# Performance work log

Measured on AMD Instinct MI355X. Metric: run time of the kernel, lower is better.

Reference implementation:

```python
import jax, jax.numpy as jnp
import numpy as np

B, N, C, H, D, K = 4, 8192, 384, 12, 2, 32
M = N // K            # 256 members per cluster
CH = C // H // 2      # 16 = q/k head dim (v gets 2*head_dim per the 6-way split)


def setup_inputs() -> dict:
    key = jax.random.key(0)
    ks = jax.random.split(key, 8)
    pos = jax.random.uniform(ks[0], (B, N, D), jnp.float32)
    feat = jax.random.normal(ks[1], (B, N, C), jnp.float32)
    # per-(b*h) row permutation of 0..N-1 -> clusters partition all tokens (cluster_mask=None path)
    perm_keys = jax.random.split(ks[2], B * H)
    member_idx = jax.vmap(lambda kk: jax.random.permutation(kk, N))(perm_keys).reshape(B * H, K, M)
    w_qkv = jax.random.normal(ks[3], (3 * C, C), jnp.float32) * (C ** -0.5)
    b_qkv = jnp.zeros((3 * C,), jnp.float32)
    w_pos = jax.random.normal(ks[4], (H, D), jnp.float32) * 0.1   # Conv1d(h*d->h, ksize 1, groups=h) weight squeezed
    b_pos = jnp.zeros((H,), jnp.float32)
    w_proj = jax.random.normal(ks[5], (C, 2 * C), jnp.float32) * ((2 * C) ** -0.5)
    b_proj = jnp.zeros((C,), jnp.float32)
    return {"pos": pos, "feat": feat, "member_idx": member_idx,
            "w_qkv": w_qkv, "b_qkv": b_qkv, "w_pos": w_pos, "b_pos": b_pos,
            "w_proj": w_proj, "b_proj": b_proj}


def reference(pos, feat, member_idx, w_qkv, b_qkv, w_pos, b_pos, w_proj, b_proj):
    b, n, c = feat.shape
    d = pos.shape[2]
    bh, k, m = member_idx.shape
    h = bh // b
    ch = c // h // 2
    scale = (c // h) ** -0.5

    # qkv projection -> (b*h, n, 6, ch)
    qkv = feat @ w_qkv.T + b_qkv                      # b n 3c
    qkv = qkv.reshape(b, n, h, 6, ch).transpose(0, 2, 1, 3, 4).reshape(bh, n, 6, ch)

    # gather cluster members -> (b*k, h, m, 6, ch)
    row = jnp.arange(bh)[:, None, None]
    g = qkv[row, member_idx]                          # bh k m 6 ch
    g = g.reshape(b, h, k, m, 6, ch).transpose(0, 2, 1, 3, 4, 5).reshape(b * k, h, m, 6, ch)
    q = g[:, :, :, 0] * scale                         # bk h m ch
    kk = g[:, :, :, 1]                                # bk h m ch
    v = g[:, :, :, 2:].reshape(b * k, h, m, 4 * ch)   # bk h m 2c_

    attn = jnp.einsum('khic,khjc->khij', q, kk)       # bk h m m (k axis = b*k)

    # positional bias: kernel-1 grouped conv is linear -> bias[i,j] = s_j - s_i + b_pos
    pos_n = pos / pos.reshape(-1, d).max(0)           # b n d
    pos_bh = jnp.repeat(pos_n, h, axis=0)             # bh n d
    pos_g = pos_bh[row, member_idx]                   # bh k m d
    pos_g = pos_g.reshape(b, h, k, m, d).transpose(0, 2, 1, 3, 4).reshape(b * k, h, m, d)
    s = jnp.einsum('khmd,hd->khm', pos_g, w_pos)      # bk h m
    pos_bias = s[:, :, None, :] - s[:, :, :, None] + b_pos[None, :, None, None]

    attn = jax.nn.softmax(attn + pos_bias, axis=-1)
    out = jnp.einsum('khij,khjc->khic', attn, v)      # bk h m 2c_

    # scatter back to original token order (member_idx is a permutation per row)
    out = out.reshape(b, k, h, m, 4 * ch).transpose(0, 2, 1, 3, 4).reshape(bh, k * m, 4 * ch)
    new_feat = jnp.zeros((bh, n, 4 * ch), out.dtype)
    new_feat = new_feat.at[jnp.arange(bh)[:, None], member_idx.reshape(bh, k * m)].set(out)
    feat2 = new_feat.reshape(b, h, n, 4 * ch).transpose(0, 2, 1, 3).reshape(b, n, 2 * c)

    return feat2 @ w_proj.T + b_proj                  # b n c
```

## Files before the change

### kernel.cpp

```cpp
#include <hip/hip_runtime.h>
#include <hip/hip_bf16.h>

#define B_  4
#define N_  8192
#define C_  384
#define H_  12
#define K_  32
#define M_  256
#define BN_ (B_*N_)
#define QKVD 1152
#define VSTR 260
#define LOG2E 1.4426950408889634f


typedef __attribute__((ext_vector_type(8)))  short  bf16x8;
typedef __attribute__((ext_vector_type(4)))  float  f32x4;
typedef __attribute__((ext_vector_type(16))) float  f32x16;
typedef __attribute__((ext_vector_type(4)))  ushort ushort4v;
typedef __attribute__((ext_vector_type(8)))  ushort ushort8v;

#define GLOBAL_AS __attribute__((address_space(1)))
#define LDS_AS    __attribute__((address_space(3)))

__device__ __forceinline__ void load_lds_16B(const ushort* g, ushort* l) {
    __builtin_amdgcn_global_load_lds((const GLOBAL_AS unsigned int*)g,
                                     (LDS_AS unsigned int*)l, 16, 0, 0);
}
__device__ __forceinline__ unsigned cvtpk_bf16(float lo, float hi) {
    unsigned r;
    asm("v_cvt_pk_bf16_f32 %0, %1, %2" : "=v"(r) : "v"(lo), "v"(hi));
    return r;
}
__device__ __forceinline__ float exp2_fast(float x) {
    float r;
    asm("v_exp_f32 %0, %1" : "=v"(r) : "v"(x));
    return r;
}
__device__ __forceinline__ float rcp_fast(float x) {
    float r;
    asm("v_rcp_f32 %0, %1" : "=v"(r) : "v"(x));
    return r;
}

#define CF_BLK 12288
#define CW_BLK 720
#define WQN 110592
#define WPN 73728
__global__ __launch_bounds__(256) void prologue_kernel(const float* __restrict__ pos,
                                                       const float* __restrict__ feat,
                                                       const float* __restrict__ wq,
                                                       const float* __restrict__ wp,
                                                       unsigned* __restrict__ pmax,
                                                       ushort* __restrict__ featb,
                                                       ushort* __restrict__ wqb,
                                                       ushort* __restrict__ wpb) {
    const int bid = blockIdx.x;
    if (bid < CF_BLK) {
        int i = bid * 256 + threadIdx.x;
        float4 a = reinterpret_cast<const float4*>(feat)[i];
        unsigned u01 = cvtpk_bf16(a.x, a.y), u23 = cvtpk_bf16(a.z, a.w);
        ushort4 o = { (ushort)(u01 & 0xffff), (ushort)(u01 >> 16),
                      (ushort)(u23 & 0xffff), (ushort)(u23 >> 16) };
        reinterpret_cast<ushort4*>(featb)[i] = o;
        return;
    }
    if (bid < CF_BLK + CW_BLK) {
        int i = (bid - CF_BLK) * 256 + threadIdx.x;
        if (i >= WQN + WPN) return;
        const float* src; ushort* dst; int j;
        if (i < WQN) { src = wq; dst = wqb; j = i; }
        else         { src = wp; dst = wpb; j = i - WQN; }
        float4 a = reinterpret_cast<const float4*>(src)[j];
        unsigned u01 = cvtpk_bf16(a.x, a.y), u23 = cvtpk_bf16(a.z, a.w);
        ushort4 o = { (ushort)(u01 & 0xffff), (ushort)(u01 >> 16),
                      (ushort)(u23 & 0xffff), (ushort)(u23 >> 16) };
        reinterpret_cast<ushort4*>(dst)[j] = o;
        return;
    }
    {
        int vb = bid - CF_BLK - CW_BLK;
        int tid = vb * 256 + threadIdx.x;
        float m0 = 0.f, m1 = 0.f;
        for (int i = tid; i < BN_; i += 8 * 256) {
            m0 = fmaxf(m0, pos[(size_t)i * 2 + 0]);
            m1 = fmaxf(m1, pos[(size_t)i * 2 + 1]);
        }
        #pragma unroll
        for (int off = 32; off; off >>= 1) {
            m0 = fmaxf(m0, __shfl_down(m0, off));
            m1 = fmaxf(m1, __shfl_down(m1, off));
        }
        __shared__ float s0[4], s1[4];
        int w = threadIdx.x >> 6;
        if ((threadIdx.x & 63) == 0) { s0[w] = m0; s1[w] = m1; }
        __syncthreads();
        if (threadIdx.x == 0) {
            for (int i = 1; i < 4; i++) { m0 = fmaxf(m0, s0[i]); m1 = fmaxf(m1, s1[i]); }
            pmax[2 * vb + 0] = __float_as_uint(m0);
            pmax[2 * vb + 1] = __float_as_uint(m1);
        }
    }
}

__global__ __launch_bounds__(512) void gemm_qkv_s(const ushort* __restrict__ A,
                                                  const ushort* __restrict__ Bw,
                                                  const float* __restrict__ bias,
                                                  ushort* __restrict__ qkv) {
    constexpr int NB = QKVD / 128;
    __shared__ ushort As[256 * 64];
    __shared__ ushort Bs[128 * 64];
    const int wgid = blockIdx.x;
    const int xcd  = wgid & 7;
    const int loc  = wgid >> 3;
    const int bm = (xcd * 16 + loc / NB) * 256;
    const int bn = (loc % NB) * 128;
    const int t = threadIdx.x;
    const int l = t & 63;
    const int wid = t >> 6;
    const int wr = wid >> 1, wc = wid & 1;
    const int fr = l & 15, fq = l >> 4;

    f32x4 zero = {0.f, 0.f, 0.f, 0.f};
    f32x4 acc[4][4];
    #pragma unroll
    for (int m = 0; m < 4; m++)
        #pragma unroll
        for (int n = 0; n < 4; n++) acc[m][n] = zero;

    for (int k0 = 0; k0 < 384; k0 += 64) {
        #pragma unroll
        for (int i = 0; i < 4; i++) {
            int elem = (i * 512 + t) * 8;
            int row = elem >> 6, kk = elem & 63;
            int kks = kk ^ ((row & 7) << 3);
            load_lds_16B(A + (size_t)(bm + row) * 384 + k0 + kks, &As[elem]);
        }
        #pragma unroll
        for (int i = 0; i < 2; i++) {
            int elem = (i * 512 + t) * 8;
            int row = elem >> 6, kk = elem & 63;
            int kks = kk ^ ((row & 7) << 3);
            load_lds_16B(Bw + (size_t)(bn + row) * 384 + k0 + kks, &Bs[elem]);
        }
        __syncthreads();
        #pragma unroll
        for (int kk = 0; kk < 64; kk += 32) {
            bf16x8 af[4], bfr[4];
            #pragma unroll
            for (int m = 0; m < 4; m++) {
                int row = wr * 64 + m * 16 + fr;
                af[m] = *reinterpret_cast<const bf16x8*>(&As[row * 64 + ((kk + fq * 8) ^ ((row & 7) << 3))]);
            }
            #pragma unroll
            for (int n = 0; n < 4; n++) {
                int row = wc * 64 + n * 16 + fr;
                bfr[n] = *reinterpret_cast<const bf16x8*>(&Bs[row * 64 + ((kk + fq * 8) ^ ((row & 7) << 3))]);
            }
            #pragma unroll
            for (int m = 0; m < 4; m++)
                #pragma unroll
                for (int n = 0; n < 4; n++)
                    acc[m][n] = __builtin_amdgcn_mfma_f32_16x16x32_bf16(af[m], bfr[n], acc[m][n], 0, 0, 0);
        }
        __syncthreads();
    }
    const int bq = bm >> 13;
    const int nbase = bm & (N_ - 1);
    #pragma unroll
    for (int n = 0; n < 4; n++) {
        int col = bn + wc * 64 + n * 16 + fr;
        int hc = col / 96, cn = col % 96;
        float bc = bias[col];
        ushort* base = qkv + ((size_t)(bq * H_ + hc) * N_ + nbase) * 96 + cn;
        #pragma unroll
        for (int m = 0; m < 4; m++) {
            #pragma unroll
            for (int r = 0; r < 4; r++) {
                int rowoff = wr * 64 + m * 16 + fq * 4 + r;
                unsigned up = cvtpk_bf16(acc[m][n][r] + bc, 0.f);
                base[(size_t)rowoff * 96] = (ushort)(up & 0xffff);
            }
        }
    }
}

__global__ __launch_bounds__(256, 2) void attn_kernel(const ushort* __restrict__ qkv,
                                                      const int* __restrict__ member_idx,
                                                      const float* __restrict__ pos,
                                                      const float* __restrict__ w_pos,
                                                      const unsigned* __restrict__ pmax_u,
                                                      ushort* __restrict__ feat2) {
    const int id = blockIdx.x;
    const int bh = (id >> 8) * 8 + (id & 7);
    const int kc = (id >> 3) & 31;
    const int b = bh / H_, h = bh % H_;
    __shared__ ushort Ks[M_ * 16];
    __shared__ ushort Vt[64 * VSTR];
    __shared__ float  SpA[M_];
    __shared__ int    Idx[M_];
    __shared__ float  dinvS[M_];

    const int t  = threadIdx.x;
    const int w  = t >> 6, l = t & 63;
    const int hi = l >> 5, ln = l & 31;
    const int* mi = member_idx + (((size_t)b * H_ + h) * K_ + kc) * M_;
    const ushort* slab = qkv + (size_t)bh * N_ * 96;
    const size_t rowbase = (size_t)b * N_;
    const float scale2 = 0.17677669529663687f * LOG2E;

    const int nq0 = mi[w * 64 + ln];
    const int nq1 = mi[w * 64 + 32 + ln];
    bf16x8 qf0 = *(const bf16x8*)(slab + (size_t)nq0 * 96 + hi * 8);
    bf16x8 qf1 = *(const bf16x8*)(slab + (size_t)nq1 * 96 + hi * 8);
    #pragma unroll
    for (int it = 0; it < 2; it++) {
        int idx = it * 256 + t;
        int row = idx >> 1, half = idx & 1;
        int n = mi[row];
        load_lds_16B(slab + (size_t)n * 96 + 16 + half * 8, &Ks[idx * 8]);
    }
    {
        int u = t >> 1, cqh = t & 1;
        int n0 = mi[2 * u], n1 = mi[2 * u + 1];
        #pragma unroll
        for (int qq = 0; qq < 2; qq++) {
            int cq = 2 * cqh + qq;
            const ushort* s0 = slab + (size_t)n0 * 96 + 32 + cq * 16;
            const ushort* s1 = slab + (size_t)n1 * 96 + 32 + cq * 16;
            union { ushort8v v; unsigned u4[4]; } v0a, v0b, v1a, v1b;
            v0a.v = *(const ushort8v*)s0;
            v0b.v = *(const ushort8v*)(s0 + 8);
            v1a.v = *(const ushort8v*)s1;
            v1b.v = *(const ushort8v*)(s1 + 8);
            #pragma unroll
            for (int iw = 0; iw < 4; iw++) {
                unsigned ea = __builtin_amdgcn_perm(v1a.u4[iw], v0a.u4[iw], 0x05040100u);
                unsigned oa = __builtin_amdgcn_perm(v1a.u4[iw], v0a.u4[iw], 0x07060302u);
                *(unsigned*)&Vt[(cq * 16 + 2 * iw)     * VSTR + 2 * u] = ea;
                *(unsigned*)&Vt[(cq * 16 + 2 * iw + 1) * VSTR + 2 * u] = oa;
                unsigned eb = __builtin_amdgcn_perm(v1b.u4[iw], v0b.u4[iw], 0x05040100u);
                unsigned ob = __builtin_amdgcn_perm(v1b.u4[iw], v0b.u4[iw], 0x07060302u);
                *(unsigned*)&Vt[(cq * 16 + 8 + 2 * iw)     * VSTR + 2 * u] = eb;
                *(unsigned*)&Vt[(cq * 16 + 8 + 2 * iw + 1) * VSTR + 2 * u] = ob;
            }
        }
    }
    {
        int n = mi[t];
        Idx[t] = n;
        float f0 = __uint_as_float(pmax_u[0]), f1 = __uint_as_float(pmax_u[1]);
        #pragma unroll
        for (int k = 1; k < 8; k++) {
            f0 = fmaxf(f0, __uint_as_float(pmax_u[2 * k + 0]));
            f1 = fmaxf(f1, __uint_as_float(pmax_u[2 * k + 1]));
        }
        float inv0 = rcp_fast(f0);
        float inv1 = rcp_fast(f1);
        float sp = pos[(rowbase + n) * 2 + 0] * inv0 * w_pos[h * 2 + 0]
                 + pos[(rowbase + n) * 2 + 1] * inv1 * w_pos[h * 2 + 1];
        int jj = t & 31, jt = t >> 5;
        int r  = (jj & 3) | ((jj >> 3) << 2);
        int hb = (jj >> 2) & 1;
        SpA[jt * 32 + hb * 16 + r] = sp * LOG2E;
    }
    __syncthreads();

    f32x16 zero16;
    #pragma unroll
    for (int i = 0; i < 16; i++) zero16[i] = 0.f;
    ushort* f2slab = feat2 + (size_t)bh * N_ * 64;

    #pragma unroll
    for (int p = 0; p < 2; p++) {
        const int qb = w * 64 + p * 32;
        const bf16x8 qf = p ? qf1 : qf0;

        f32x16 sac[8];
        __builtin_amdgcn_s_setprio(1);
        #pragma unroll
        for (int jt = 0; jt < 8; jt++) {
            bf16x8 kf = *(const bf16x8*)&Ks[(32 * jt + ln) * 16 + hi * 8];
            sac[jt] = __builtin_amdgcn_mfma_f32_32x32x16_bf16(kf, qf, zero16, 0, 0, 0);
        }
        __builtin_amdgcn_s_setprio(0);

        float mx = -3.0e38f;
        #pragma unroll
        for (int jt = 0; jt < 8; jt++) {
            f32x4 bia[4];
            #pragma unroll
            for (int q4 = 0; q4 < 4; q4++)
                bia[q4] = *(const f32x4*)&SpA[jt * 32 + hi * 16 + q4 * 4];
            #pragma unroll
            for (int r = 0; r < 16; r++)
                sac[jt][r] = fmaf(sac[jt][r], scale2, bia[r >> 2][r & 3]);
            #pragma unroll
            for (int r = 0; r < 16; r += 2)
                mx = fmaxf(mx, fmaxf(sac[jt][r], sac[jt][r + 1]));
        }
        mx = fmaxf(mx, __shfl_xor(mx, 32));
        float sum = 0.f;
        #pragma unroll
        for (int jt = 0; jt < 8; jt++)
            #pragma unroll
            for (int r = 0; r < 16; r++) {
                float pv = exp2_fast(sac[jt][r] - mx);
                sac[jt][r] = pv;
                sum += pv;
            }
        sum += __shfl_xor(sum, 32);
        float inv = rcp_fast(sum);
        if (hi == 0) dinvS[qb + ln] = inv;

        f32x16 oa0 = zero16, oa1 = zero16;
        __builtin_amdgcn_s_setprio(1);
        #pragma unroll
        for (int g = 0; g < 16; g++) {
            const int jt = g >> 1, hf = (g & 1) * 8;
            unsigned a0 = cvtpk_bf16(sac[jt][hf + 0], sac[jt][hf + 1]);
            unsigned a1 = cvtpk_bf16(sac[jt][hf + 2], sac[jt][hf + 3]);
            unsigned b0 = cvtpk_bf16(sac[jt][hf + 4], sac[jt][hf + 5]);
            unsigned b1 = cvtpk_bf16(sac[jt][hf + 6], sac[jt][hf + 7]);
            asm("v_permlane32_swap_b32 %0, %1" : "+v"(a0), "+v"(b0));
            asm("v_permlane32_swap_b32 %0, %1" : "+v"(a1), "+v"(b1));
            union { unsigned uu[4]; bf16x8 v; } pa;
            pa.uu[0] = a0; pa.uu[1] = a1; pa.uu[2] = b0; pa.uu[3] = b1;
            union { ushort4v hv[2]; bf16x8 v; } vf0, vf1;
            vf0.hv[0] = *(const ushort4v*)&Vt[ln * VSTR + g * 16 + hi * 8];
            vf0.hv[1] = *(const ushort4v*)&Vt[ln * VSTR + g * 16 + hi * 8 + 4];
            vf1.hv[0] = *(const ushort4v*)&Vt[(ln + 32) * VSTR + g * 16 + hi * 8];
            vf1.hv[1] = *(const ushort4v*)&Vt[(ln + 32) * VSTR + g * 16 + hi * 8 + 4];
            oa0 = __builtin_amdgcn_mfma_f32_32x32x16_bf16(pa.v, vf0.v, oa0, 0, 0, 0);
            oa1 = __builtin_amdgcn_mfma_f32_32x32x16_bf16(pa.v, vf1.v, oa1, 0, 0, 0);
        }
        __builtin_amdgcn_s_setprio(0);

        #pragma unroll
        for (int r = 0; r < 16; r++) {
            int crow = (r & 3) + 8 * (r >> 2) + 4 * hi;
            float dv = dinvS[qb + crow];
            int ni = Idx[qb + crow];
            unsigned up = cvtpk_bf16(oa0[r] * dv, oa1[r] * dv);
            ushort* dst = f2slab + (size_t)ni * 64 + ln;
            dst[0]  = (ushort)(up & 0xffff);
            dst[32] = (ushort)(up >> 16);
        }
    }
}

__global__ __launch_bounds__(512) void gemm_proj_s(const ushort* __restrict__ A,
                                                   const ushort* __restrict__ Bw,
                                                   const float* __restrict__ bias,
                                                   float* __restrict__ Cout) {
    constexpr int NB = C_ / 128;
    __shared__ ushort As[256 * 64];
    __shared__ ushort Bs[128 * 64];
    const int wgid = blockIdx.x;
    const int xcd  = wgid & 7;
    const int loc  = wgid >> 3;
    const int bm = (xcd * 16 + loc / NB) * 256;
    const int bn = (loc % NB) * 128;
    const int t = threadIdx.x;
    const int l = t & 63;
    const int wid = t >> 6;
    const int wr = wid >> 1, wc = wid & 1;
    const int fr = l & 15, fq = l >> 4;
    const int bq = bm >> 13;
    const int nbase = bm & (N_ - 1);

    f32x4 zero = {0.f, 0.f, 0.f, 0.f};
    f32x4 acc[4][4];
    #pragma unroll
    for (int m = 0; m < 4; m++)
        #pragma unroll
        for (int n = 0; n < 4; n++) acc[m][n] = zero;

    for (int k0 = 0; k0 < 768; k0 += 64) {
        const ushort* Aslab = A + ((size_t)(bq * H_ + (k0 >> 6)) * N_ + nbase) * 64;
        #pragma unroll
        for (int i = 0; i < 4; i++) {
            int elem = (i * 512 + t) * 8;
            int row = elem >> 6, kk = elem & 63;
            int kks = kk ^ ((row & 7) << 3);
            load_lds_16B(Aslab + (size_t)row * 64 + kks, &As[elem]);
        }
        #pragma unroll
        for (int i = 0; i < 2; i++) {
            int elem = (i * 512 + t) * 8;
            int row = elem >> 6, kk = elem & 63;
            int kks = kk ^ ((row & 7) << 3);
            load_lds_16B(Bw + (size_t)(bn + row) * 768 + k0 + kks, &Bs[elem]);
        }
        __syncthreads();
        #pragma unroll
        for (int kk = 0; kk < 64; kk += 32) {
            bf16x8 af[4], bfr[4];
            #pragma unroll
            for (int m = 0; m < 4; m++) {
                int row = wr * 64 + m * 16 + fr;
                af[m] = *reinterpret_cast<const bf16x8*>(&As[row * 64 + ((kk + fq * 8) ^ ((row & 7) << 3))]);
            }
            #pragma unroll
            for (int n = 0; n < 4; n++) {
                int row = wc * 64 + n * 16 + fr;
                bfr[n] = *reinterpret_cast<const bf16x8*>(&Bs[row * 64 + ((kk + fq * 8) ^ ((row & 7) << 3))]);
            }
            #pragma unroll
            for (int m = 0; m < 4; m++)
                #pragma unroll
                for (int n = 0; n < 4; n++)
                    acc[m][n] = __builtin_amdgcn_mfma_f32_16x16x32_bf16(af[m], bfr[n], acc[m][n], 0, 0, 0);
        }
        __syncthreads();
    }
    #pragma unroll
    for (int n = 0; n < 4; n++) {
        int col = bn + wc * 64 + n * 16 + fr;
        float bc = bias[col];
        #pragma unroll
        for (int m = 0; m < 4; m++) {
            #pragma unroll
            for (int r = 0; r < 4; r++) {
                size_t row = bm + wr * 64 + m * 16 + fq * 4 + r;
                Cout[row * C_ + col] = acc[m][n][r] + bc;
            }
        }
    }
}

extern "C" void kernel_launch(void* const* d_in, const int* in_sizes, int n_in,
                              void* d_out, int out_size, void* d_ws, size_t ws_size,
                              hipStream_t stream) {
    const float* pos    = (const float*)d_in[0];
    const float* feat   = (const float*)d_in[1];
    const int*   midx   = (const int*)  d_in[2];
    const float* w_qkv  = (const float*)d_in[3];
    const float* b_qkv  = (const float*)d_in[4];
    const float* w_pos  = (const float*)d_in[5];
    const float* b_pos  = (const float*)d_in[6];  (void)b_pos;
    const float* w_proj = (const float*)d_in[7];
    const float* b_proj = (const float*)d_in[8];
    float* out = (float*)d_out;

    char* ws = (char*)d_ws;
    unsigned* pmax  = (unsigned*)ws;
    ushort*   qkv   = (ushort*)(ws + 256);
    ushort*   wproj = (ushort*)(ws + 256 + 75497472);
    char*     region = ws + 256 + 75497472 + 589824;
    ushort*   featb = (ushort*)region;
    ushort*   wqkvb = (ushort*)(region + 25165824);
    ushort*   feat2 = (ushort*)region;

    prologue_kernel<<<CF_BLK + CW_BLK + 8, 256, 0, stream>>>(pos, feat, w_qkv, w_proj,
                                                             pmax, featb, wqkvb, wproj);
    gemm_qkv_s<<<8 * 16 * (QKVD / 128), 512, 0, stream>>>(featb, wqkvb, b_qkv, qkv);
    attn_kernel<<<6 * 256, 256, 0, stream>>>(qkv, midx, pos, w_pos, pmax, feat2);
    gemm_proj_s<<<8 * 16 * (C_ / 128), 512, 0, stream>>>(feat2, wproj, b_proj, out);
}
```

Measured before the change: 136.3 us.

## Recompute QK scores in second pass to drop score registers and raise occupancy

The attention kernel no longer keeps all 8 score tiles (128 floats per lane) live across the softmax. It runs a first pass of QK MFMAs to find the row max, then recomputes the scores tile by tile, exponentiating and feeding each tile straight into the PV MFMAs. Launch bounds go from 2 to 3 blocks per CU, which the lower register pressure is meant to allow. The cost is doubling the QK MFMAs and the K/bias LDS reads, traded for more waves to hide latency.

```diff
diff --git a/kernel.cpp b/kernel.cpp
--- a/kernel.cpp
+++ b/kernel.cpp
@@ -184,7 +184,7 @@
     }
 }
 
-__global__ __launch_bounds__(256, 2) void attn_kernel(const ushort* __restrict__ qkv,
+__global__ __launch_bounds__(256, 3) void attn_kernel(const ushort* __restrict__ qkv,
                                                       const int* __restrict__ member_idx,
                                                       const float* __restrict__ pos,
                                                       const float* __restrict__ w_pos,
@@ -275,65 +275,67 @@
         const int qb = w * 64 + p * 32;
         const bf16x8 qf = p ? qf1 : qf0;
 
-        f32x16 sac[8];
-        __builtin_amdgcn_s_setprio(1);
+        float mx = -3.0e38f;
         #pragma unroll
         for (int jt = 0; jt < 8; jt++) {
             bf16x8 kf = *(const bf16x8*)&Ks[(32 * jt + ln) * 16 + hi * 8];
-            sac[jt] = __builtin_amdgcn_mfma_f32_32x32x16_bf16(kf, qf, zero16, 0, 0, 0);
-        }
-        __builtin_amdgcn_s_setprio(0);
-
-        float mx = -3.0e38f;
-        #pragma unroll
-        for (int jt = 0; jt < 8; jt++) {
+            f32x16 s = __builtin_amdgcn_mfma_f32_32x32x16_bf16(kf, qf, zero16, 0, 0, 0);
             f32x4 bia[4];
             #pragma unroll
             for (int q4 = 0; q4 < 4; q4++)
                 bia[q4] = *(const f32x4*)&SpA[jt * 32 + hi * 16 + q4 * 4];
             #pragma unroll
             for (int r = 0; r < 16; r++)
-                sac[jt][r] = fmaf(sac[jt][r], scale2, bia[r >> 2][r & 3]);
+                s[r] = fmaf(s[r], scale2, bia[r >> 2][r & 3]);
             #pragma unroll
             for (int r = 0; r < 16; r += 2)
-                mx = fmaxf(mx, fmaxf(sac[jt][r], sac[jt][r + 1]));
+                mx = fmaxf(mx, fmaxf(s[r], s[r + 1]));
         }
         mx = fmaxf(mx, __shfl_xor(mx, 32));
+
         float sum = 0.f;
-        #pragma unroll
-        for (int jt = 0; jt < 8; jt++)
+        f32x16 oa0 = zero16, oa1 = zero16;
+        #pragma unroll
+        for (int jt = 0; jt < 8; jt++) {
+            bf16x8 kf = *(const bf16x8*)&Ks[(32 * jt + ln) * 16 + hi * 8];
+            asm volatile("" : "+v"(kf));
+            f32x16 s = __builtin_amdgcn_mfma_f32_32x32x16_bf16(kf, qf, zero16, 0, 0, 0);
+            f32x4 bia[4];
+            #pragma unroll
+            for (int q4 = 0; q4 < 4; q4++)
+                bia[q4] = *(const f32x4*)&SpA[jt * 32 + hi * 16 + q4 * 4];
             #pragma unroll
             for (int r = 0; r < 16; r++) {
-                float pv = exp2_fast(sac[jt][r] - mx);
-                sac[jt][r] = pv;
+                float pv = exp2_fast(fmaf(s[r], scale2, bia[r >> 2][r & 3]) - mx);
+                s[r] = pv;
                 sum += pv;
             }
+            __builtin_amdgcn_s_setprio(1);
+            #pragma unroll
+            for (int half = 0; half < 2; half++) {
+                const int hf = half * 8;
+                unsigned a0 = cvtpk_bf16(s[hf + 0], s[hf + 1]);
+                unsigned a1 = cvtpk_bf16(s[hf + 2], s[hf + 3]);
+                unsigned b0 = cvtpk_bf16(s[hf + 4], s[hf + 5]);
+                unsigned b1 = cvtpk_bf16(s[hf + 6], s[hf + 7]);
+                asm("v_permlane32_swap_b32 %0, %1" : "+v"(a0), "+v"(b0));
+                asm("v_permlane32_swap_b32 %0, %1" : "+v"(a1), "+v"(b1));
+                union { unsigned uu[4]; bf16x8 v; } pa;
+                pa.uu[0] = a0; pa.uu[1] = a1; pa.uu[2] = b0; pa.uu[3] = b1;
+                const int mo = (jt * 2 + half) * 16 + hi * 8;
+                union { ushort4v hv[2]; bf16x8 v; } vf0, vf1;
+                vf0.hv[0] = *(const ushort4v*)&Vt[ln * VSTR + mo];
+                vf0.hv[1] = *(const ushort4v*)&Vt[ln * VSTR + mo + 4];
+                vf1.hv[0] = *(const ushort4v*)&Vt[(ln + 32) * VSTR + mo];
+                vf1.hv[1] = *(const ushort4v*)&Vt[(ln + 32) * VSTR + mo + 4];
+                oa0 = __builtin_amdgcn_mfma_f32_32x32x16_bf16(pa.v, vf0.v, oa0, 0, 0, 0);
+                oa1 = __builtin_amdgcn_mfma_f32_32x32x16_bf16(pa.v, vf1.v, oa1, 0, 0, 0);
+            }
+            __builtin_amdgcn_s_setprio(0);
+        }
         sum += __shfl_xor(sum, 32);
         float inv = rcp_fast(sum);
         if (hi == 0) dinvS[qb + ln] = inv;
-
-        f32x16 oa0 = zero16, oa1 = zero16;
-        __builtin_amdgcn_s_setprio(1);
-        #pragma unroll
-        for (int g = 0; g < 16; g++) {
-            const int jt = g >> 1, hf = (g & 1) * 8;
-            unsigned a0 = cvtpk_bf16(sac[jt][hf + 0], sac[jt][hf + 1]);
-            unsigned a1 = cvtpk_bf16(sac[jt][hf + 2], sac[jt][hf + 3]);
-            unsigned b0 = cvtpk_bf16(sac[jt][hf + 4], sac[jt][hf + 5]);
-            unsigned b1 = cvtpk_bf16(sac[jt][hf + 6], sac[jt][hf + 7]);
-            asm("v_permlane32_swap_b32 %0, %1" : "+v"(a0), "+v"(b0));
-            asm("v_permlane32_swap_b32 %0, %1" : "+v"(a1), "+v"(b1));
-            union { unsigned uu[4]; bf16x8 v; } pa;
-            pa.uu[0] = a0; pa.uu[1] = a1; pa.uu[2] = b0; pa.uu[3] = b1;
-            union { ushort4v hv[2]; bf16x8 v; } vf0, vf1;
-            vf0.hv[0] = *(const ushort4v*)&Vt[ln * VSTR + g * 16 + hi * 8];
-            vf0.hv[1] = *(const ushort4v*)&Vt[ln * VSTR + g * 16 + hi * 8 + 4];
-            vf1.hv[0] = *(const ushort4v*)&Vt[(ln + 32) * VSTR + g * 16 + hi * 8];
-            vf1.hv[1] = *(const ushort4v*)&Vt[(ln + 32) * VSTR + g * 16 + hi * 8 + 4];
-            oa0 = __builtin_amdgcn_mfma_f32_32x32x16_bf16(pa.v, vf0.v, oa0, 0, 0, 0);
-            oa1 = __builtin_amdgcn_mfma_f32_32x32x16_bf16(pa.v, vf1.v, oa1, 0, 0, 0);
-        }
-        __builtin_amdgcn_s_setprio(0);
 
         #pragma unroll
         for (int r = 0; r < 16; r++) {
```

Result: faster. 133.2 us (median of 2 runs) (-2.3%).
